# Kernel tuning notes

Hardware: AMD Instinct MI355X
Metric: run time of the kernel (lower is better)

## Reference

```python
import jax, jax.numpy as jnp
import numpy as np

DIM_V, DIM_T, DIM_OUT, NUM_HEADS = 1024, 1024, 1024, 16
HEAD_DIM = DIM_OUT // NUM_HEADS
BETA = 1.0  # module multiplies scores by self.beta (=1); self.scale is unused


def setup_inputs() -> dict:
    key = jax.random.key(0)
    ks = jax.random.split(key, 12)
    B, N1, N2 = 8, 256, 4096
    E = jax.random.normal(ks[0], (B, N1, DIM_T), dtype=jnp.float32)
    I = jax.random.normal(ks[1], (B, N2, DIM_V), dtype=jnp.float32)
    s = 0.02
    # Conv1d(kernel_size=1) == linear; weights stored [out, in], bias [out]
    q_w = jax.random.normal(ks[2], (DIM_OUT, DIM_T), dtype=jnp.float32) * s
    q_b = jnp.zeros((DIM_OUT,), dtype=jnp.float32)
    k_w = jax.random.normal(ks[3], (DIM_OUT, DIM_V), dtype=jnp.float32) * s
    k_b = jnp.zeros((DIM_OUT,), dtype=jnp.float32)
    v_w = jax.random.normal(ks[4], (DIM_OUT, DIM_V), dtype=jnp.float32) * s
    v_b = jnp.zeros((DIM_OUT,), dtype=jnp.float32)
    p_w = jax.random.normal(ks[5], (DIM_OUT, DIM_OUT), dtype=jnp.float32) * s
    p_b = jnp.zeros((DIM_OUT,), dtype=jnp.float32)
    return {"E": E, "I": I, "q_w": q_w, "q_b": q_b, "k_w": k_w, "k_b": k_b,
            "v_w": v_w, "v_b": v_b, "p_w": p_w, "p_b": p_b}


def reference(E, I, q_w, q_b, k_w, k_b, v_w, v_b, p_w, p_b):
    B, N1, _ = E.shape
    _, N2, _ = I.shape
    # 1x1 conv projections == dense layers over channel dim
    Q = (jnp.einsum('bnc,oc->bno', E, q_w) + q_b).reshape(B, N1, NUM_HEADS, HEAD_DIM)
    K = (jnp.einsum('bmc,oc->bmo', I, k_w) + k_b).reshape(B, N2, NUM_HEADS, HEAD_DIM)
    V = (jnp.einsum('bmc,oc->bmo', I, v_w) + v_b).reshape(B, N2, NUM_HEADS, HEAD_DIM)
    # cross-attention scores [B, H, N1, N2]
    attn = jnp.einsum('bnhd,bmhd->bhnm', Q, K) * BETA
    attn = jax.nn.softmax(attn, axis=-1)
    U = jnp.einsum('bhnm,bmhd->bnhd', attn, V).reshape(B, N1, DIM_OUT)
    U = jnp.einsum('bnc,oc->bno', U, p_w) + p_b
    U = U / jnp.linalg.norm(U, axis=-1, keepdims=True)
    return jnp.concatenate([E, U], axis=2)  # [B, N1, dim_t + dim_out]
```

## Files before the change

### kernel.cpp

```cpp
#include <hip/hip_runtime.h>
#include <hip/hip_bf16.h>
#include <stdint.h>


typedef __bf16 bf16_t;
typedef __attribute__((ext_vector_type(8))) __bf16 bf16x8;
typedef __attribute__((ext_vector_type(4))) __bf16 bf16x4;
typedef __attribute__((ext_vector_type(4))) float f32x4;

#define DEVINL __device__ __forceinline__

DEVINL f32x4 mfma16(bf16x8 a, bf16x8 b, f32x4 c) {
  return __builtin_amdgcn_mfma_f32_16x16x32_bf16(a, b, c, 0, 0, 0);
}

DEVINL float fexp2(float x) { return __builtin_exp2f(x); }

DEVINL bf16x8 load8(const bf16_t* p) { return *(const bf16x8*)p; }
DEVINL bf16x8 load8(const float* p) {
  const float4 u = *(const float4*)p;
  const float4 v = *(const float4*)(p + 4);
  bf16x8 r;
  r[0] = (bf16_t)u.x; r[1] = (bf16_t)u.y; r[2] = (bf16_t)u.z; r[3] = (bf16_t)u.w;
  r[4] = (bf16_t)v.x; r[5] = (bf16_t)v.y; r[6] = (bf16_t)v.z; r[7] = (bf16_t)v.w;
  return r;
}

DEVINL uint32_t pack_bf16(float a, float b) {
  union { bf16_t h[2]; uint32_t u; } x;
  x.h[0] = (bf16_t)a; x.h[1] = (bf16_t)b;
  return x.u;
}

DEVINL void async16(const void* g, void* l) {
  typedef const __attribute__((address_space(1))) unsigned int* gp1;
  typedef __attribute__((address_space(3))) unsigned int* lp3;
  __builtin_amdgcn_global_load_lds((gp1)(uintptr_t)g,
                                   (lp3)(uint32_t)(uintptr_t)l, 16, 0, 0);
}

__global__ __launch_bounds__(256) void cvt_f32_bf16(
    const float* __restrict__ src, bf16_t* __restrict__ dst, int n8) {
  const int i = blockIdx.x * 256 + threadIdx.x;
  if (i < n8) *(bf16x8*)(dst + (size_t)i * 8) = load8(src + (size_t)i * 8);
}

template <int MODE>
__global__ __launch_bounds__(256) void gemm_bt_async(
    const bf16_t* __restrict__ A, const bf16_t* __restrict__ B,
    const float* __restrict__ bias, bf16_t* __restrict__ C,
    int M, int N, int K) {
  __shared__ bf16_t As[2][128 * 32];
  __shared__ bf16_t Bs[2][128 * 32];
  const int tid = threadIdx.x;
  const int w = tid >> 6, lane = tid & 63, quad = lane >> 4, l16 = lane & 15;
  const int bid = blockIdx.x;
  const int swz = (bid & 7) * (int)(gridDim.x >> 3) + (bid >> 3);
  const int big = swz >> 3, small = swz & 7;
  const int bm = 128 * (MODE == 1 ? small : big);
  const int bn = 128 * (MODE == 1 ? big : small);
  const int wm = (w & 1) * 64, wn = (w >> 1) * 64;
  const int srow = tid >> 2;
  const int sw8 = ((tid & 3) ^ (srow & 3)) * 8;

  const bf16_t* Ag0 = A + (size_t)(bm + srow) * K + sw8;
  const bf16_t* Ag1 = Ag0 + (size_t)64 * K;
  const bf16_t* Bg0 = B + (size_t)(bn + srow) * K + sw8;
  const bf16_t* Bg1 = Bg0 + (size_t)64 * K;

  f32x4 acc[4][4] = {};

  for (int k0 = 0; k0 < K; k0 += 64) {
    async16(Ag0 + k0, As[0] + tid * 8);
    async16(Ag1 + k0, As[0] + 64 * 32 + tid * 8);
    async16(Bg0 + k0, Bs[0] + tid * 8);
    async16(Bg1 + k0, Bs[0] + 64 * 32 + tid * 8);
    async16(Ag0 + k0 + 32, As[1] + tid * 8);
    async16(Ag1 + k0 + 32, As[1] + 64 * 32 + tid * 8);
    async16(Bg0 + k0 + 32, Bs[1] + tid * 8);
    async16(Bg1 + k0 + 32, Bs[1] + 64 * 32 + tid * 8);
    __syncthreads();
#pragma unroll
    for (int h = 0; h < 2; h++) {
      bf16x8 af[4], bfr[4];
#pragma unroll
      for (int mt = 0; mt < 4; mt++) {
        const int r = wm + mt * 16 + l16;
        af[mt] = *(const bf16x8*)(As[h] + r * 32 + ((quad ^ (r & 3)) * 8));
      }
#pragma unroll
      for (int nt = 0; nt < 4; nt++) {
        const int r = wn + nt * 16 + l16;
        bfr[nt] = *(const bf16x8*)(Bs[h] + r * 32 + ((quad ^ (r & 3)) * 8));
      }
#pragma unroll
      for (int mt = 0; mt < 4; mt++)
#pragma unroll
        for (int nt = 0; nt < 4; nt++)
          acc[mt][nt] = mfma16(af[mt], bfr[nt], acc[mt][nt]);
    }
    __syncthreads();
  }

#pragma unroll
  for (int mt = 0; mt < 4; mt++) {
#pragma unroll
    for (int nt = 0; nt < 4; nt++) {
      const int gm0 = bm + wm + mt * 16 + quad * 4;
      const int gn = bn + wn + nt * 16 + l16;
#pragma unroll
      for (int r = 0; r < 4; r++) {
        const int gm = gm0 + r;
        C[(size_t)gm * N + gn] =
            (bf16_t)(acc[mt][nt][r] + bias[MODE == 1 ? gm : gn]);
      }
    }
  }
}

template <int MODE, typename TA, typename TB>
__global__ __launch_bounds__(256) void gemm_bt_reg(
    const TA* __restrict__ A, const TB* __restrict__ B,
    const float* __restrict__ bias, void* __restrict__ Cv,
    int M, int N, int K) {
  __shared__ bf16_t As[128 * 32];
  __shared__ bf16_t Bs[128 * 32];
  const int tid = threadIdx.x;
  const int w = tid >> 6, lane = tid & 63, quad = lane >> 4, l16 = lane & 15;
  const int bm = blockIdx.x * 128, bn = blockIdx.y * 128;
  const int wm = (w & 1) * 64, wn = (w >> 1) * 64;
  const int srow = tid >> 2;
  const int swz = ((tid & 3) ^ (srow & 3)) * 8;

  const TA* Ag0 = A + (size_t)(bm + srow) * K + swz;
  const TA* Ag1 = Ag0 + (size_t)64 * K;
  const TB* Bg0 = B + (size_t)(bn + srow) * K + swz;
  const TB* Bg1 = Bg0 + (size_t)64 * K;
  bf16_t* Al0 = As + tid * 8;
  bf16_t* Al1 = As + 64 * 32 + tid * 8;
  bf16_t* Bl0 = Bs + tid * 8;
  bf16_t* Bl1 = Bs + 64 * 32 + tid * 8;

  f32x4 acc[4][4] = {};

  for (int k0 = 0; k0 < K; k0 += 32) {
    const bf16x8 a0 = load8(Ag0 + k0);
    const bf16x8 a1 = load8(Ag1 + k0);
    const bf16x8 b0 = load8(Bg0 + k0);
    const bf16x8 b1 = load8(Bg1 + k0);
    *(bf16x8*)Al0 = a0;
    *(bf16x8*)Al1 = a1;
    *(bf16x8*)Bl0 = b0;
    *(bf16x8*)Bl1 = b1;
    __syncthreads();
    bf16x8 af[4], bfr[4];
#pragma unroll
    for (int mt = 0; mt < 4; mt++) {
      const int r = wm + mt * 16 + l16;
      af[mt] = *(const bf16x8*)(As + r * 32 + ((quad ^ (r & 3)) * 8));
    }
#pragma unroll
    for (int nt = 0; nt < 4; nt++) {
      const int r = wn + nt * 16 + l16;
      bfr[nt] = *(const bf16x8*)(Bs + r * 32 + ((quad ^ (r & 3)) * 8));
    }
#pragma unroll
    for (int mt = 0; mt < 4; mt++)
#pragma unroll
      for (int nt = 0; nt < 4; nt++)
        acc[mt][nt] = mfma16(af[mt], bfr[nt], acc[mt][nt]);
    __syncthreads();
  }

#pragma unroll
  for (int mt = 0; mt < 4; mt++) {
#pragma unroll
    for (int nt = 0; nt < 4; nt++) {
      const int gm0 = bm + wm + mt * 16 + quad * 4;
      const int gn = bn + wn + nt * 16 + l16;
#pragma unroll
      for (int r = 0; r < 4; r++) {
        const int gm = gm0 + r;
        float v = acc[mt][nt][r] + bias[MODE == 1 ? gm : gn];
        if (MODE == 3) v *= 1.4426950408889634f;
        if (MODE == 2)
          ((float*)Cv)[(size_t)gm * N + gn] = v;
        else
          ((bf16_t*)Cv)[(size_t)gm * N + gn] = (bf16_t)v;
      }
    }
  }
}

DEVINL void loadK(const bf16_t* p, bf16x8& e0, bf16x8& e1, bf16x8& o0,
                  bf16x8& o1) {
  e0 = *(const bf16x8*)(p);
  e1 = *(const bf16x8*)(p + 32);
  o0 = *(const bf16x8*)(p + 16 * 1024);
  o1 = *(const bf16x8*)(p + 16 * 1024 + 32);
}

DEVINL void loadV(const bf16_t* p, bf16x8& v0, bf16x8& v1, bf16x8& v2,
                  bf16x8& v3) {
  union { bf16x4 h4[2]; bf16x8 v; } u0, u1, u2, u3;
  u0.h4[0] = *(const bf16x4*)(p);
  u0.h4[1] = *(const bf16x4*)(p + 16);
  u1.h4[0] = *(const bf16x4*)(p + (size_t)16 * 32768);
  u1.h4[1] = *(const bf16x4*)(p + (size_t)16 * 32768 + 16);
  u2.h4[0] = *(const bf16x4*)(p + (size_t)32 * 32768);
  u2.h4[1] = *(const bf16x4*)(p + (size_t)32 * 32768 + 16);
  u3.h4[0] = *(const bf16x4*)(p + (size_t)48 * 32768);
  u3.h4[1] = *(const bf16x4*)(p + (size_t)48 * 32768 + 16);
  v0 = u0.v; v1 = u1.v; v2 = u2.v; v3 = u3.v;
}

DEVINL void attn_step(bf16x8 ke0, bf16x8 ke1, bf16x8 ko0, bf16x8 ko1,
                      bf16x8 v0, bf16x8 v1, bf16x8 v2, bf16x8 v3,
                      const bf16x8 (&qf0)[4], const bf16x8 (&qf1)[4],
                      f32x4 (&o)[4][4], float (&lacc)[4]) {
  const f32x4 cm44 = {-44.f, -44.f, -44.f, -44.f};
#pragma unroll
  for (int qg = 0; qg < 4; qg++) {
    f32x4 z0 = cm44;
    z0 = mfma16(ke0, qf0[qg], z0);
    const f32x4 ste = mfma16(ke1, qf1[qg], z0);
    f32x4 z1 = cm44;
    z1 = mfma16(ko0, qf0[qg], z1);
    const f32x4 sto = mfma16(ko1, qf1[qg], z1);
    const float pe0 = fexp2(ste[0]), pe1 = fexp2(ste[1]);
    const float pe2 = fexp2(ste[2]), pe3 = fexp2(ste[3]);
    const float po0 = fexp2(sto[0]), po1 = fexp2(sto[1]);
    const float po2 = fexp2(sto[2]), po3 = fexp2(sto[3]);
    lacc[qg] += ((pe0 + pe1) + (pe2 + pe3)) + ((po0 + po1) + (po2 + po3));
    union { uint32_t u[4]; bf16x8 v; } pb;
    pb.u[0] = pack_bf16(pe0, pe1);
    pb.u[1] = pack_bf16(pe2, pe3);
    pb.u[2] = pack_bf16(po0, po1);
    pb.u[3] = pack_bf16(po2, po3);
    o[0][qg] = mfma16(v0, pb.v, o[0][qg]);
    o[1][qg] = mfma16(v1, pb.v, o[1][qg]);
    o[2][qg] = mfma16(v2, pb.v, o[2][qg]);
    o[3][qg] = mfma16(v3, pb.v, o[3][qg]);
  }
}

__global__ __launch_bounds__(256) void attn_regs(
    const bf16_t* __restrict__ QU, const bf16_t* __restrict__ Kbuf,
    const bf16_t* __restrict__ Vtbuf, float* __restrict__ opart,
    float* __restrict__ mls) {
  __shared__ float lo[128 * 68];
  __shared__ float ll[2][128];
  const int tid = threadIdx.x;
  const int w = tid >> 6, lane = tid & 63, quad = lane >> 4, l16 = lane & 15;
  const int wq = w >> 1, wk = w & 1;
  const int flat = blockIdx.x;
  const int qt = flat >> 9, s = (flat >> 7) & 3, h = (flat >> 3) & 15, b = flat & 7;

  bf16x8 qf0[4], qf1[4];
  const bf16_t* qb =
      QU + (size_t)(b * 256 + qt * 128 + wq * 64 + l16) * 1024 + h * 64 + quad * 8;
#pragma unroll
  for (int qg = 0; qg < 4; qg++) {
    qf0[qg] = *(const bf16x8*)(qb + (size_t)qg * 16 * 1024);
    qf1[qg] = *(const bf16x8*)(qb + (size_t)qg * 16 * 1024 + 32);
  }

  const bf16_t* kg =
      Kbuf + (size_t)(b * 4096 + s * 1024 + wk * 32 + l16) * 1024 + h * 64 + quad * 8;
  const bf16_t* vg =
      Vtbuf + (size_t)(h * 64 + l16) * 32768 + b * 4096 + s * 1024 + wk * 32 + quad * 4;

  f32x4 o[4][4] = {};
  float lacc[4] = {};

  bf16x8 kae0, kae1, kao0, kao1, kbe0, kbe1, kbo0, kbo1;
  bf16x8 va0, va1, va2, va3, vb0, vb1, vb2, vb3;
  loadK(kg, kae0, kae1, kao0, kao1);

#pragma unroll 1
  for (int it = 0; it < 16; it += 2) {
    loadV(vg, va0, va1, va2, va3);
    kg += 64 * 1024;
    loadK(kg, kbe0, kbe1, kbo0, kbo1);
    attn_step(kae0, kae1, kao0, kao1, va0, va1, va2, va3, qf0, qf1, o, lacc);
    vg += 64;
    loadV(vg, vb0, vb1, vb2, vb3);
    kg += 64 * 1024;
    if (it < 14)
      loadK(kg, kae0, kae1, kao0, kao1);
    attn_step(kbe0, kbe1, kbo0, kbo1, vb0, vb1, vb2, vb3, qf0, qf1, o, lacc);
    vg += 64;
  }

#pragma unroll
  for (int qg = 0; qg < 4; qg++) {
    lacc[qg] += __shfl_xor(lacc[qg], 16);
    lacc[qg] += __shfl_xor(lacc[qg], 32);
  }
  if (quad == 0) {
#pragma unroll
    for (int qg = 0; qg < 4; qg++) ll[wk][wq * 64 + qg * 16 + l16] = lacc[qg];
  }
  if (wk == 0) {
#pragma unroll
    for (int qg = 0; qg < 4; qg++)
#pragma unroll
      for (int dt = 0; dt < 4; dt++)
        *(f32x4*)&lo[(wq * 64 + qg * 16 + l16) * 68 + dt * 16 + quad * 4] =
            o[dt][qg];
  }
  __syncthreads();
  if (wk == 1) {
    const int pr0 = ((b * 16 + h) << 8) | (qt * 128 + wq * 64);
#pragma unroll
    for (int qg = 0; qg < 4; qg++) {
      const int q = wq * 64 + qg * 16 + l16;
      const int pr = pr0 + qg * 16 + l16;
#pragma unroll
      for (int dt = 0; dt < 4; dt++) {
        f32x4 t = *(const f32x4*)&lo[q * 68 + dt * 16 + quad * 4];
        t = t + o[dt][qg];
        *(f32x4*)(opart + ((size_t)s * 32768 + pr) * 64 + dt * 16 + quad * 4) = t;
      }
      if (quad == 0) mls[(size_t)s * 32768 + pr] = ll[0][q] + ll[1][q];
    }
  }
}

__global__ __launch_bounds__(256) void attn_combine(
    const float* __restrict__ opart, const float* __restrict__ mls,
    bf16_t* __restrict__ QU) {
  const int w = threadIdx.x >> 6, lane = threadIdx.x & 63;
  const int pr = blockIdx.x * 4 + w;
  float L = 0.f, acc = 0.f;
#pragma unroll
  for (int s = 0; s < 4; s++) {
    L += mls[(size_t)s * 32768 + pr];
    acc += opart[((size_t)s * 32768 + pr) * 64 + lane];
  }
  const int b = pr >> 12, h = (pr >> 8) & 15, q = pr & 255;
  QU[(size_t)(b * 256 + q) * 1024 + h * 64 + lane] =
      (bf16_t)(acc / fmaxf(L, 1e-37f));
}

__global__ __launch_bounds__(256) void attn_old(
    bf16_t* QU, const bf16_t* __restrict__ Kbuf,
    const bf16_t* __restrict__ Vtbuf, int hg, int G, int Kst) {
  __shared__ bf16_t Ks[64 * 64];
  __shared__ bf16_t Vs[64 * 64];
  __shared__ bf16_t Ps[4][16 * 64];
  const int tid = threadIdx.x;
  const int w = tid >> 6, lane = tid & 63, quad = lane >> 4, l16 = lane & 15;
  const int flat = blockIdx.x;
  const int qt = flat / (8 * G);
  const int rem = flat - qt * 8 * G;
  const int hh = rem % G, b = rem / G;
  const int h = hg + hh;

  const int qrow = b * 256 + qt * 64 + w * 16 + l16;
  const bf16_t* qbase = QU + (size_t)qrow * 1024 + h * 64 + quad * 8;
  const bf16x8 qf0 = *(const bf16x8*)(qbase);
  const bf16x8 qf1 = *(const bf16x8*)(qbase + 32);

  const int srow = tid >> 3;
  const int swz = ((tid & 7) ^ (srow & 7)) * 8;
  const bf16_t* Kg = Kbuf + (size_t)(b * 4096 + srow) * Kst + hh * 64 + swz;
  const bf16_t* Vg = Vtbuf + (size_t)(hh * 64 + srow) * 32768 + b * 4096 + swz;

  f32x4 o[4] = {};
  float mrow[4] = {-1e30f, -1e30f, -1e30f, -1e30f};
  float lrow[4] = {0.f, 0.f, 0.f, 0.f};
  const float L2E = 1.4426950408889634f;

  bf16x8 kv0 = *(const bf16x8*)(Kg);
  bf16x8 kv1 = *(const bf16x8*)(Kg + (size_t)32 * Kst);
  bf16x8 vv0 = *(const bf16x8*)(Vg);
  bf16x8 vv1 = *(const bf16x8*)(Vg + (size_t)32 * 32768);

  for (int kt = 0; kt < 64; kt++) {
    __syncthreads();
    *(bf16x8*)(Ks + tid * 8) = kv0;
    *(bf16x8*)(Ks + 32 * 64 + tid * 8) = kv1;
    *(bf16x8*)(Vs + tid * 8) = vv0;
    *(bf16x8*)(Vs + 32 * 64 + tid * 8) = vv1;
    __syncthreads();
    if (kt < 63) {
      const size_t ko = (size_t)(kt + 1) * 64;
      kv0 = *(const bf16x8*)(Kg + ko * Kst);
      kv1 = *(const bf16x8*)(Kg + (ko + 32) * Kst);
      vv0 = *(const bf16x8*)(Vg + ko);
      vv1 = *(const bf16x8*)(Vg + ko + (size_t)32 * 32768);
    }

    f32x4 s[4];
#pragma unroll
    for (int nt = 0; nt < 4; nt++) {
      const int key = nt * 16 + l16;
      const bf16x8 kf0 = *(const bf16x8*)(Ks + key * 64 + ((quad ^ (key & 7)) * 8));
      const bf16x8 kf1 = *(const bf16x8*)(Ks + key * 64 + (((quad + 4) ^ (key & 7)) * 8));
      f32x4 z = {0.f, 0.f, 0.f, 0.f};
      z = mfma16(qf0, kf0, z);
      s[nt] = mfma16(qf1, kf1, z);
    }

    float mnew[4], alpha[4], rsum[4];
#pragma unroll
    for (int r = 0; r < 4; r++) {
      float mx = fmaxf(fmaxf(s[0][r], s[1][r]), fmaxf(s[2][r], s[3][r]));
      mx = fmaxf(mx, __shfl_xor(mx, 1));
      mx = fmaxf(mx, __shfl_xor(mx, 2));
      mx = fmaxf(mx, __shfl_xor(mx, 4));
      mx = fmaxf(mx, __shfl_xor(mx, 8));
      mnew[r] = fmaxf(mrow[r], mx);
      alpha[r] = exp2f((mrow[r] - mnew[r]) * L2E);
      rsum[r] = 0.f;
    }
#pragma unroll
    for (int nt = 0; nt < 4; nt++) {
      const int key = nt * 16 + l16;
#pragma unroll
      for (int r = 0; r < 4; r++) {
        const float p = exp2f((s[nt][r] - mnew[r]) * L2E);
        rsum[r] += p;
        const int q = quad * 4 + r;
        Ps[w][q * 64 + (((key >> 3) ^ (q & 7)) * 8) + (key & 7)] = (bf16_t)p;
      }
    }
#pragma unroll
    for (int r = 0; r < 4; r++) {
      rsum[r] += __shfl_xor(rsum[r], 1);
      rsum[r] += __shfl_xor(rsum[r], 2);
      rsum[r] += __shfl_xor(rsum[r], 4);
      rsum[r] += __shfl_xor(rsum[r], 8);
      lrow[r] = lrow[r] * alpha[r] + rsum[r];
      mrow[r] = mnew[r];
    }
#pragma unroll
    for (int nt = 0; nt < 4; nt++) {
      o[nt][0] *= alpha[0]; o[nt][1] *= alpha[1];
      o[nt][2] *= alpha[2]; o[nt][3] *= alpha[3];
    }

    __syncthreads();

    const bf16x8 pf0 = *(const bf16x8*)(&Ps[w][l16 * 64 + ((quad ^ (l16 & 7)) * 8)]);
    const bf16x8 pf1 = *(const bf16x8*)(&Ps[w][l16 * 64 + (((quad + 4) ^ (l16 & 7)) * 8)]);
#pragma unroll
    for (int nt = 0; nt < 4; nt++) {
      const int d = nt * 16 + l16;
      const bf16x8 vf0 = *(const bf16x8*)(Vs + d * 64 + ((quad ^ (d & 7)) * 8));
      const bf16x8 vf1 = *(const bf16x8*)(Vs + d * 64 + (((quad + 4) ^ (d & 7)) * 8));
      o[nt] = mfma16(pf0, vf0, o[nt]);
      o[nt] = mfma16(pf1, vf1, o[nt]);
    }
  }

  float inv[4];
#pragma unroll
  for (int r = 0; r < 4; r++) inv[r] = 1.0f / fmaxf(lrow[r], 1e-30f);
#pragma unroll
  for (int nt = 0; nt < 4; nt++) {
#pragma unroll
    for (int r = 0; r < 4; r++) {
      const int row = b * 256 + qt * 64 + w * 16 + quad * 4 + r;
      QU[(size_t)row * 1024 + h * 64 + nt * 16 + l16] = (bf16_t)(o[nt][r] * inv[r]);
    }
  }
}

__global__ __launch_bounds__(256) void norm_concat(
    const float* __restrict__ E, const float* __restrict__ P,
    float* __restrict__ out) {
  const int row = blockIdx.x, tid = threadIdx.x;
  const int w = tid >> 6, lane = tid & 63;

  *(float4*)(out + (size_t)row * 2048 + tid * 4) =
      *(const float4*)(E + (size_t)row * 1024 + tid * 4);

  const float4 p = *(const float4*)(P + (size_t)row * 1024 + tid * 4);
  float ss = p.x * p.x + p.y * p.y + p.z * p.z + p.w * p.w;
#pragma unroll
  for (int m = 1; m <= 32; m <<= 1) ss += __shfl_xor(ss, m);
  __shared__ float red[4];
  if (lane == 0) red[w] = ss;
  __syncthreads();
  const float rn = rsqrtf(fmaxf(red[0] + red[1] + red[2] + red[3], 1e-30f));
  float4 q;
  q.x = p.x * rn; q.y = p.y * rn; q.z = p.z * rn; q.w = p.w * rn;
  *(float4*)(out + (size_t)row * 2048 + 1024 + tid * 4) = q;
}

extern "C" void kernel_launch(void* const* d_in, const int* in_sizes, int n_in,
                              void* d_out, int out_size, void* d_ws, size_t ws_size,
                              hipStream_t stream) {
  (void)in_sizes; (void)n_in; (void)out_size;
  const float* E   = (const float*)d_in[0];
  const float* I   = (const float*)d_in[1];
  const float* q_w = (const float*)d_in[2];
  const float* q_b = (const float*)d_in[3];
  const float* k_w = (const float*)d_in[4];
  const float* k_b = (const float*)d_in[5];
  const float* v_w = (const float*)d_in[6];
  const float* v_b = (const float*)d_in[7];
  const float* p_w = (const float*)d_in[8];
  const float* p_b = (const float*)d_in[9];
  float* out = (float*)d_out;
  char* ws = (char*)d_ws;

  if (ws_size >= (200ull << 20)) {
    bf16_t* QU    = (bf16_t*)(ws);
    bf16_t* k_wbf = (bf16_t*)(ws + (4u << 20));
    bf16_t* v_wbf = (bf16_t*)(ws + (6u << 20));
    bf16_t* Ibf   = (bf16_t*)(ws + (8u << 20));
    float*  Pf    = (float*)(ws + (8u << 20));
    float*  opart = (float*)(ws + (16u << 20));
    float*  mls   = (float*)(ws + (52u << 20));
    bf16_t* Kbuf  = (bf16_t*)(ws + (72u << 20));
    bf16_t* Vtbuf = (bf16_t*)(ws + (136u << 20));

    cvt_f32_bf16<<<16384, 256, 0, stream>>>(I, Ibf, 32768 * 1024 / 8);
    cvt_f32_bf16<<<512, 256, 0, stream>>>(k_w, k_wbf, 1024 * 1024 / 8);
    cvt_f32_bf16<<<512, 256, 0, stream>>>(v_w, v_wbf, 1024 * 1024 / 8);

    gemm_bt_reg<3, float, float><<<dim3(16, 8), 256, 0, stream>>>(
        E, q_w, q_b, QU, 2048, 1024, 1024);
    gemm_bt_async<0><<<2048, 256, 0, stream>>>(
        Ibf, k_wbf, k_b, Kbuf, 32768, 1024, 1024);
    gemm_bt_async<1><<<2048, 256, 0, stream>>>(
        v_wbf, Ibf, v_b, Vtbuf, 1024, 32768, 1024);
    attn_regs<<<1024, 256, 0, stream>>>(QU, Kbuf, Vtbuf, opart, mls);
    attn_combine<<<8192, 256, 0, stream>>>(opart, mls, QU);
    gemm_bt_reg<2, bf16_t, float><<<dim3(16, 8), 256, 0, stream>>>(
        QU, p_w, p_b, Pf, 2048, 1024, 1024);
    norm_concat<<<2048, 256, 0, stream>>>(E, Pf, out);
  } else {
    int G = 2;
    if (ws_size >= (133ull << 20)) G = 16;
    else if (ws_size >= (69ull << 20)) G = 8;
    else if (ws_size >= (37ull << 20)) G = 4;
    bf16_t* QU    = (bf16_t*)(ws);
    bf16_t* Kbuf  = (bf16_t*)(ws + (4u << 20));
    bf16_t* Vtbuf = (bf16_t*)(ws + (4u << 20) + ((size_t)G << 22));
    float*  Pf    = (float*)(ws + (4u << 20));

    gemm_bt_reg<0, float, float><<<dim3(16, 8), 256, 0, stream>>>(
        E, q_w, q_b, QU, 2048, 1024, 1024);
    for (int hg = 0; hg < 16; hg += G) {
      const int Nh = G * 64;
      gemm_bt_reg<0, float, float><<<dim3(256, Nh / 128), 256, 0, stream>>>(
          I, k_w + (size_t)hg * 64 * 1024, k_b + hg * 64, Kbuf, 32768, Nh, 1024);
      gemm_bt_reg<1, float, float><<<dim3(Nh / 128, 256), 256, 0, stream>>>(
          v_w + (size_t)hg * 64 * 1024, I, v_b + hg * 64, Vtbuf, Nh, 32768, 1024);
      attn_old<<<32 * G, 256, 0, stream>>>(QU, Kbuf, Vtbuf, hg, G, Nh);
    }
    gemm_bt_reg<2, bf16_t, float><<<dim3(16, 8), 256, 0, stream>>>(
        QU, p_w, p_b, Pf, 2048, 1024, 1024);
    norm_concat<<<2048, 256, 0, stream>>>(E, Pf, out);
  }
}
```

Measured before the change: 590.2 us.

## Stage K/V tiles in swizzled shared memory with 512-thread attention blocks

The attention kernel now moves from per-wave register loads of K and V straight from global memory to cooperative async copies of 128-key K and V tiles into XOR-swizzled LDS. Those tiles are shared by 8 waves, each covering 32 queries instead of 64. The aim is to cut redundant global/L2 traffic, since several waves previously re-read the same K/V, and to raise occupancy by using fewer registers per wave. In exchange it adds two block barriers per iteration and drops the previous software register prefetch, so loads are no longer overlapped with compute inside a block.

```diff
diff --git a/kernel.cpp b/kernel.cpp
--- a/kernel.cpp
+++ b/kernel.cpp
@@ -192,35 +192,13 @@
   }
 }
 
-DEVINL void loadK(const bf16_t* p, bf16x8& e0, bf16x8& e1, bf16x8& o0,
-                  bf16x8& o1) {
-  e0 = *(const bf16x8*)(p);
-  e1 = *(const bf16x8*)(p + 32);
-  o0 = *(const bf16x8*)(p + 16 * 1024);
-  o1 = *(const bf16x8*)(p + 16 * 1024 + 32);
-}
-
-DEVINL void loadV(const bf16_t* p, bf16x8& v0, bf16x8& v1, bf16x8& v2,
-                  bf16x8& v3) {
-  union { bf16x4 h4[2]; bf16x8 v; } u0, u1, u2, u3;
-  u0.h4[0] = *(const bf16x4*)(p);
-  u0.h4[1] = *(const bf16x4*)(p + 16);
-  u1.h4[0] = *(const bf16x4*)(p + (size_t)16 * 32768);
-  u1.h4[1] = *(const bf16x4*)(p + (size_t)16 * 32768 + 16);
-  u2.h4[0] = *(const bf16x4*)(p + (size_t)32 * 32768);
-  u2.h4[1] = *(const bf16x4*)(p + (size_t)32 * 32768 + 16);
-  u3.h4[0] = *(const bf16x4*)(p + (size_t)48 * 32768);
-  u3.h4[1] = *(const bf16x4*)(p + (size_t)48 * 32768 + 16);
-  v0 = u0.v; v1 = u1.v; v2 = u2.v; v3 = u3.v;
-}
-
-DEVINL void attn_step(bf16x8 ke0, bf16x8 ke1, bf16x8 ko0, bf16x8 ko1,
-                      bf16x8 v0, bf16x8 v1, bf16x8 v2, bf16x8 v3,
-                      const bf16x8 (&qf0)[4], const bf16x8 (&qf1)[4],
-                      f32x4 (&o)[4][4], float (&lacc)[4]) {
+DEVINL void attn_step2(bf16x8 ke0, bf16x8 ke1, bf16x8 ko0, bf16x8 ko1,
+                       const bf16x8 (&vf)[4],
+                       const bf16x8 (&qf0)[2], const bf16x8 (&qf1)[2],
+                       f32x4 (&o)[4][2], float (&lacc)[2]) {
   const f32x4 cm44 = {-44.f, -44.f, -44.f, -44.f};
 #pragma unroll
-  for (int qg = 0; qg < 4; qg++) {
+  for (int qg = 0; qg < 2; qg++) {
     f32x4 z0 = cm44;
     z0 = mfma16(ke0, qf0[qg], z0);
     const f32x4 ste = mfma16(ke1, qf1[qg], z0);
@@ -237,84 +215,109 @@
     pb.u[1] = pack_bf16(pe2, pe3);
     pb.u[2] = pack_bf16(po0, po1);
     pb.u[3] = pack_bf16(po2, po3);
-    o[0][qg] = mfma16(v0, pb.v, o[0][qg]);
-    o[1][qg] = mfma16(v1, pb.v, o[1][qg]);
-    o[2][qg] = mfma16(v2, pb.v, o[2][qg]);
-    o[3][qg] = mfma16(v3, pb.v, o[3][qg]);
-  }
-}
-
-__global__ __launch_bounds__(256) void attn_regs(
+    o[0][qg] = mfma16(vf[0], pb.v, o[0][qg]);
+    o[1][qg] = mfma16(vf[1], pb.v, o[1][qg]);
+    o[2][qg] = mfma16(vf[2], pb.v, o[2][qg]);
+    o[3][qg] = mfma16(vf[3], pb.v, o[3][qg]);
+  }
+}
+
+__global__ __launch_bounds__(512, 4) void attn_regs(
     const bf16_t* __restrict__ QU, const bf16_t* __restrict__ Kbuf,
     const bf16_t* __restrict__ Vtbuf, float* __restrict__ opart,
     float* __restrict__ mls) {
-  __shared__ float lo[128 * 68];
-  __shared__ float ll[2][128];
+  __shared__ __attribute__((aligned(16))) char smem[35840];
+  bf16_t* Ks = (bf16_t*)smem;
+  bf16_t* Vs = (bf16_t*)(smem + 16384);
+  float* lo = (float*)smem;
+  float* ll = (float*)(smem + 34816);
   const int tid = threadIdx.x;
   const int w = tid >> 6, lane = tid & 63, quad = lane >> 4, l16 = lane & 15;
-  const int wq = w >> 1, wk = w & 1;
+  const int wq = w >> 1, wk = w & 1, xr = l16 & 7;
   const int flat = blockIdx.x;
   const int qt = flat >> 9, s = (flat >> 7) & 3, h = (flat >> 3) & 15, b = flat & 7;
 
-  bf16x8 qf0[4], qf1[4];
+  bf16x8 qf0[2], qf1[2];
   const bf16_t* qb =
-      QU + (size_t)(b * 256 + qt * 128 + wq * 64 + l16) * 1024 + h * 64 + quad * 8;
-#pragma unroll
-  for (int qg = 0; qg < 4; qg++) {
+      QU + (size_t)(b * 256 + qt * 128 + wq * 32 + l16) * 1024 + h * 64 + quad * 8;
+#pragma unroll
+  for (int qg = 0; qg < 2; qg++) {
     qf0[qg] = *(const bf16x8*)(qb + (size_t)qg * 16 * 1024);
     qf1[qg] = *(const bf16x8*)(qb + (size_t)qg * 16 * 1024 + 32);
   }
 
-  const bf16_t* kg =
-      Kbuf + (size_t)(b * 4096 + s * 1024 + wk * 32 + l16) * 1024 + h * 64 + quad * 8;
-  const bf16_t* vg =
-      Vtbuf + (size_t)(h * 64 + l16) * 32768 + b * 4096 + s * 1024 + wk * 32 + quad * 4;
-
-  f32x4 o[4][4] = {};
-  float lacc[4] = {};
-
-  bf16x8 kae0, kae1, kao0, kao1, kbe0, kbe1, kbo0, kbo1;
-  bf16x8 va0, va1, va2, va3, vb0, vb1, vb2, vb3;
-  loadK(kg, kae0, kae1, kao0, kao1);
-
-#pragma unroll 1
-  for (int it = 0; it < 16; it += 2) {
-    loadV(vg, va0, va1, va2, va3);
-    kg += 64 * 1024;
-    loadK(kg, kbe0, kbe1, kbo0, kbo1);
-    attn_step(kae0, kae1, kao0, kao1, va0, va1, va2, va3, qf0, qf1, o, lacc);
-    vg += 64;
-    loadV(vg, vb0, vb1, vb2, vb3);
-    kg += 64 * 1024;
-    if (it < 14)
-      loadK(kg, kae0, kae1, kao0, kao1);
-    attn_step(kbe0, kbe1, kbo0, kbo1, vb0, vb1, vb2, vb3, qf0, qf1, o, lacc);
-    vg += 64;
-  }
-
-#pragma unroll
-  for (int qg = 0; qg < 4; qg++) {
+  const int krow = tid >> 3;
+  const int ksc = (tid & 7) ^ (krow & 7);
+  const int vrow = tid >> 4;
+  const int vsc = (tid & 15) ^ (vrow & 7);
+  const bf16_t* ksrc0 =
+      Kbuf + (size_t)(b * 4096 + s * 1024 + krow) * 1024 + h * 64 + ksc * 8;
+  const bf16_t* ksrc1 = ksrc0 + (size_t)64 * 1024;
+  const bf16_t* vsrc0 =
+      Vtbuf + (size_t)(h * 64 + vrow) * 32768 + b * 4096 + s * 1024 + vsc * 8;
+  const bf16_t* vsrc1 = vsrc0 + (size_t)32 * 32768;
+
+  f32x4 o[4][2] = {};
+  float lacc[2] = {};
+
+  for (int it = 0; it < 8; it++) {
+    async16(ksrc0, Ks + tid * 8);
+    async16(ksrc1, Ks + 4096 + tid * 8);
+    async16(vsrc0, Vs + tid * 8);
+    async16(vsrc1, Vs + 4096 + tid * 8);
+    ksrc0 += (size_t)128 * 1024;
+    ksrc1 += (size_t)128 * 1024;
+    vsrc0 += 128;
+    vsrc1 += 128;
+    __syncthreads();
+#pragma unroll
+    for (int sub = 0; sub < 2; sub++) {
+      const int rowe = wk * 64 + sub * 32 + l16, rowo = rowe + 16;
+      const bf16x8 ke0 = *(const bf16x8*)(Ks + rowe * 64 + ((quad ^ xr) * 8));
+      const bf16x8 ke1 =
+          *(const bf16x8*)(Ks + rowe * 64 + (((quad + 4) ^ xr) * 8));
+      const bf16x8 ko0 = *(const bf16x8*)(Ks + rowo * 64 + ((quad ^ xr) * 8));
+      const bf16x8 ko1 =
+          *(const bf16x8*)(Ks + rowo * 64 + (((quad + 4) ^ xr) * 8));
+      bf16x8 vf[4];
+      const int c8 = wk * 8 + sub * 4 + (quad >> 1), in4 = (quad & 1) * 4;
+#pragma unroll
+      for (int dt = 0; dt < 4; dt++) {
+        const int vr = dt * 16 + l16;
+        union { bf16x4 h4[2]; bf16x8 v; } u;
+        u.h4[0] = *(const bf16x4*)(Vs + vr * 128 + ((c8 ^ xr) * 8) + in4);
+        u.h4[1] =
+            *(const bf16x4*)(Vs + vr * 128 + (((c8 + 2) ^ xr) * 8) + in4);
+        vf[dt] = u.v;
+      }
+      attn_step2(ke0, ke1, ko0, ko1, vf, qf0, qf1, o, lacc);
+    }
+    __syncthreads();
+  }
+
+#pragma unroll
+  for (int qg = 0; qg < 2; qg++) {
     lacc[qg] += __shfl_xor(lacc[qg], 16);
     lacc[qg] += __shfl_xor(lacc[qg], 32);
   }
   if (quad == 0) {
 #pragma unroll
-    for (int qg = 0; qg < 4; qg++) ll[wk][wq * 64 + qg * 16 + l16] = lacc[qg];
+    for (int qg = 0; qg < 2; qg++) ll[wk * 128 + wq * 32 + qg * 16 + l16] = lacc[qg];
   }
   if (wk == 0) {
 #pragma unroll
-    for (int qg = 0; qg < 4; qg++)
+    for (int qg = 0; qg < 2; qg++)
 #pragma unroll
       for (int dt = 0; dt < 4; dt++)
-        *(f32x4*)&lo[(wq * 64 + qg * 16 + l16) * 68 + dt * 16 + quad * 4] =
+        *(f32x4*)&lo[(wq * 32 + qg * 16 + l16) * 68 + dt * 16 + quad * 4] =
             o[dt][qg];
   }
   __syncthreads();
   if (wk == 1) {
-    const int pr0 = ((b * 16 + h) << 8) | (qt * 128 + wq * 64);
-#pragma unroll
-    for (int qg = 0; qg < 4; qg++) {
-      const int q = wq * 64 + qg * 16 + l16;
+    const int pr0 = ((b * 16 + h) << 8) | (qt * 128 + wq * 32);
+#pragma unroll
+    for (int qg = 0; qg < 2; qg++) {
+      const int q = wq * 32 + qg * 16 + l16;
       const int pr = pr0 + qg * 16 + l16;
 #pragma unroll
       for (int dt = 0; dt < 4; dt++) {
@@ -322,7 +325,7 @@
         t = t + o[dt][qg];
         *(f32x4*)(opart + ((size_t)s * 32768 + pr) * 64 + dt * 16 + quad * 4) = t;
       }
-      if (quad == 0) mls[(size_t)s * 32768 + pr] = ll[0][q] + ll[1][q];
+      if (quad == 0) mls[(size_t)s * 32768 + pr] = ll[q] + ll[128 + q];
     }
   }
 }
@@ -528,7 +531,7 @@
         Ibf, k_wbf, k_b, Kbuf, 32768, 1024, 1024);
     gemm_bt_async<1><<<2048, 256, 0, stream>>>(
         v_wbf, Ibf, v_b, Vtbuf, 1024, 32768, 1024);
-    attn_regs<<<1024, 256, 0, stream>>>(QU, Kbuf, Vtbuf, opart, mls);
+    attn_regs<<<1024, 512, 0, stream>>>(QU, Kbuf, Vtbuf, opart, mls);
     attn_combine<<<8192, 256, 0, stream>>>(opart, mls, QU);
     gemm_bt_reg<2, bf16_t, float><<<dim3(16, 8), 256, 0, stream>>>(
         QU, p_w, p_b, Pf, 2048, 1024, 1024);
```

After: 559.5 us. -5.2%, faster.
